# Kernel tuning notes

Hardware: AMD Instinct MI355X
Metric: run time of the kernel (lower is better)

## Reference

```python
import jax, jax.numpy as jnp
import numpy as np

D_MODEL = 1024
D_INNER = 2048   # expand=2
D_STATE = 16
D_CONV = 4
DT_RANK = 64     # ceil(d_model/16)
BATCH = 4
SEQLEN = 2048


def setup_inputs() -> dict:
    key = jax.random.key(0)
    ks = jax.random.split(key, 9)
    f = lambda k, shape, s=0.02: jax.random.normal(k, shape, dtype=jnp.float32) * s
    return {
        "x": jax.random.normal(ks[0], (BATCH, SEQLEN, D_MODEL), dtype=jnp.float32),
        "norm_w": jnp.ones((D_MODEL,), jnp.float32),
        "in_proj_w": f(ks[1], (2 * D_INNER, D_MODEL)),
        "conv_w": f(ks[2], (D_INNER, D_CONV), 0.1),
        "conv_b": f(ks[3], (D_INNER,), 0.1),
        "x_proj_w": f(ks[4], (DT_RANK + 2 * D_STATE, D_INNER)),
        "dt_proj_w": f(ks[5], (D_INNER, DT_RANK), 0.1),
        "dt_proj_b": f(ks[6], (D_INNER,), 0.1),
        "A_log": jnp.log(jnp.tile(jnp.arange(1, D_STATE + 1, dtype=jnp.float32), (D_INNER, 1))),
        "D_param": jnp.ones((D_INNER,), jnp.float32),
        "out_proj_w": f(ks[7], (D_MODEL, D_INNER)),
    }


def _rmsnorm(x, w):
    eps = jnp.finfo(jnp.float32).eps
    var = jnp.mean(x * x, axis=-1, keepdims=True)
    return x * jax.lax.rsqrt(var + eps) * w


def _mamba(x_norm, in_proj_w, conv_w, conv_b, x_proj_w,
           dt_proj_w, dt_proj_b, A_log, D_param, out_proj_w):
    B, L, _ = x_norm.shape
    # input projection -> [B, L, 2*D_INNER], split into x and gate z
    xz = jnp.einsum('bld,ed->ble', x_norm, in_proj_w)
    x_in, z = jnp.split(xz, 2, axis=-1)
    # causal depthwise conv1d (kernel D_CONV, left pad D_CONV-1)
    x_c = jax.lax.conv_general_dilated(
        x_in.transpose(0, 2, 1),                 # [B, D_INNER, L]
        conv_w[:, None, :],                      # [D_INNER, 1, D_CONV]
        window_strides=(1,), padding=[(D_CONV - 1, 0)],
        dimension_numbers=('NCH', 'OIH', 'NCH'),
        feature_group_count=D_INNER,
    ) + conv_b[None, :, None]
    u = jax.nn.silu(x_c.transpose(0, 2, 1))      # [B, L, D_INNER]
    # SSM parameters
    x_dbl = jnp.einsum('bld,ed->ble', u, x_proj_w)  # [B, L, DT_RANK+2*D_STATE]
    dt, B_mat, C_mat = jnp.split(x_dbl, [DT_RANK, DT_RANK + D_STATE], axis=-1)
    dt = jax.nn.softplus(jnp.einsum('blr,dr->bld', dt, dt_proj_w) + dt_proj_b)  # [B,L,D_INNER]
    A = -jnp.exp(A_log)                          # [D_INNER, D_STATE]

    # selective scan over time; state h: [B, D_INNER, D_STATE]
    def step(h, inputs):
        dt_t, B_t, C_t, u_t = inputs             # [B,Dn],[B,S],[B,S],[B,Dn]
        dA = jnp.exp(dt_t[:, :, None] * A)       # [B, Dn, S]
        h = dA * h + (dt_t * u_t)[:, :, None] * B_t[:, None, :]
        y_t = jnp.einsum('bds,bs->bd', h, C_t)
        return h, y_t

    h0 = jnp.zeros((B, D_INNER, D_STATE), x_norm.dtype)
    xs = (dt.transpose(1, 0, 2), B_mat.transpose(1, 0, 2),
          C_mat.transpose(1, 0, 2), u.transpose(1, 0, 2))
    _, ys = jax.lax.scan(step, h0, xs)           # [L, B, D_INNER]
    y = ys.transpose(1, 0, 2) + D_param * u
    y = y * jax.nn.silu(z)
    return jnp.einsum('bld,ed->ble', y, out_proj_w)  # [B, L, D_MODEL]


def reference(x, norm_w, in_proj_w, conv_w, conv_b, x_proj_w,
              dt_proj_w, dt_proj_b, A_log, D_param, out_proj_w):
    x_norm = _rmsnorm(x, norm_w)
    out = _mamba(x_norm, in_proj_w, conv_w, conv_b, x_proj_w,
                 dt_proj_w, dt_proj_b, A_log, D_param, out_proj_w)
    return x + out
```

## Files before the change

kernel.cpp:

```cpp
#include <hip/hip_runtime.h>
#include <hip/hip_bf16.h>
#include <math.h>

#define DM 1024
#define DI 2048
#define DS 16
#define DC 4
#define DR 64
#define NB 4
#define SL 2048
#define BL (NB * SL)
#define DXP (DR + 2 * DS)
#define NC 32
#define CL (SL / NC)

typedef __hip_bfloat16 bf16;
typedef __attribute__((ext_vector_type(8))) short short8;
typedef __attribute__((ext_vector_type(4))) float floatx4;
typedef unsigned int u32;

__device__ __forceinline__ float to_f(float v) { return v; }
__device__ __forceinline__ float to_f(bf16 v) { return __bfloat162float(v); }
template <typename T> __device__ __forceinline__ T from_f(float v);
template <> __device__ __forceinline__ float from_f<float>(float v) { return v; }
template <> __device__ __forceinline__ bf16 from_f<bf16>(float v) { return __float2bfloat16(v); }

__device__ __forceinline__ float bfbits2f(unsigned short u) {
  u32 b = ((u32)u) << 16;
  return __builtin_bit_cast(float, b);
}
__device__ __forceinline__ short f2bfbits(float v) {
  bf16 b = __float2bfloat16(v);
  return __builtin_bit_cast(short, b);
}
__device__ __forceinline__ float fsilu(float v) {
  return v * __builtin_amdgcn_rcpf(1.f + __expf(-v));
}

__device__ __forceinline__ void gload16(const ushort* g, ushort* l) {
  __builtin_amdgcn_global_load_lds((const __attribute__((address_space(1))) void*)g,
                                   (__attribute__((address_space(3))) void*)l,
                                   16, 0, 0);
}

__global__ __launch_bounds__(256) void f2b_k(const float* __restrict__ src,
                                             bf16* __restrict__ dst, int n) {
  int i = blockIdx.x * 256 + threadIdx.x;
  if (i < n) dst[i] = from_f<bf16>(src[i]);
}

__global__ __launch_bounds__(256) void rmsnorm_k(const float* __restrict__ x,
                                                 const float* __restrict__ w,
                                                 bf16* __restrict__ o) {
  int row = blockIdx.x;
  const float* xr = x + (size_t)row * DM;
  float ss = 0.f;
  for (int i = threadIdx.x; i < DM; i += 256) { float v = xr[i]; ss += v * v; }
  for (int off = 32; off > 0; off >>= 1) ss += __shfl_down(ss, off);
  __shared__ float sred[4];
  __shared__ float sscale;
  if ((threadIdx.x & 63) == 0) sred[threadIdx.x >> 6] = ss;
  __syncthreads();
  if (threadIdx.x == 0) {
    float t = sred[0] + sred[1] + sred[2] + sred[3];
    sscale = rsqrtf(t / (float)DM + 1.1920929e-7f);
  }
  __syncthreads();
  float sc = sscale;
  bf16* orow = o + (size_t)row * DM;
  for (int i = threadIdx.x; i < DM; i += 256) orow[i] = from_f<bf16>(xr[i] * sc * w[i]);
}

#define TM 128
#define TN 128
#define TK 32
#define LDK 40
template <int MODE>
__global__ __launch_bounds__(256) void gemm_mfma(const bf16* __restrict__ A,
                                                 const bf16* __restrict__ W,
                                                 int M, int N, int K,
                                                 bf16* __restrict__ Cx,
                                                 bf16* __restrict__ Cz, int nsplit,
                                                 float* __restrict__ Cf,
                                                 const float* __restrict__ R,
                                                 const float* __restrict__ bias) {
  __shared__ ushort Asm[TM][TK];
  __shared__ ushort Bsm[TN][TK];
  int bm = blockIdx.y * TM, bn = blockIdx.x * TN;
  int tid = threadIdx.x;
  int lane = tid & 63, wave = tid >> 6;
  int wm = (wave & 1) * 64, wn = (wave >> 1) * 64;
  int row15 = lane & 15, quad = lane >> 4;

  int srow = lane >> 2;
  int scol = (lane & 3) * 8;
  int s0 = wave * 2, s1 = wave * 2 + 1;

  const ushort* Au = (const ushort*)A;
  const ushort* Wu = (const ushort*)W;
  const ushort* ag0 = Au + (size_t)(bm + s0 * 16 + srow) * K + scol;
  const ushort* ag1 = Au + (size_t)(bm + s1 * 16 + srow) * K + scol;
  const ushort* bg0 = Wu + (size_t)(bn + s0 * 16 + srow) * K + scol;
  const ushort* bg1 = Wu + (size_t)(bn + s1 * 16 + srow) * K + scol;
  ushort* la0 = &Asm[s0 * 16][0];
  ushort* la1 = &Asm[s1 * 16][0];
  ushort* lb0 = &Bsm[s0 * 16][0];
  ushort* lb1 = &Bsm[s1 * 16][0];

  floatx4 acc[4][4] = {};

  for (int k0 = 0; k0 < K; k0 += TK) {
    gload16(ag0 + k0, la0);
    gload16(ag1 + k0, la1);
    gload16(bg0 + k0, lb0);
    gload16(bg1 + k0, lb1);
    __syncthreads();
    short8 a_f[4], b_f[4];
#pragma unroll
    for (int i = 0; i < 4; ++i)
      a_f[i] = *(const short8*)&Asm[wm + i * 16 + row15][quad * 8];
#pragma unroll
    for (int j = 0; j < 4; ++j)
      b_f[j] = *(const short8*)&Bsm[wn + j * 16 + row15][quad * 8];
#pragma unroll
    for (int i = 0; i < 4; ++i)
#pragma unroll
      for (int j = 0; j < 4; ++j)
        acc[i][j] = __builtin_amdgcn_mfma_f32_16x16x32_bf16(a_f[i], b_f[j], acc[i][j], 0, 0, 0);
    __syncthreads();
  }
#pragma unroll
  for (int mi = 0; mi < 4; ++mi) {
#pragma unroll
    for (int ni = 0; ni < 4; ++ni) {
#pragma unroll
      for (int reg = 0; reg < 4; ++reg) {
        int grow = bm + wm + mi * 16 + quad * 4 + reg;
        int gcol = bn + wn + ni * 16 + row15;
        float v = acc[mi][ni][reg];
        if (MODE == 1) {
          if (gcol < nsplit) {
            Cx[(size_t)grow * DI + gcol] = from_f<bf16>(v);
          } else {
            Cz[(size_t)grow * DI + (gcol - nsplit)] = from_f<bf16>(fsilu(v));
          }
        } else if (MODE == 2) {
          size_t o = (size_t)grow * N + gcol;
          Cf[o] = v + R[o];
        } else {
          float t = v + bias[gcol];
          float sp = (t > 20.f) ? t : __logf(1.f + __expf(t));
          Cx[(size_t)grow * N + gcol] = from_f<bf16>(sp);
        }
      }
    }
  }
}

#define XKS 128
__global__ __launch_bounds__(256) void xproj_k(const bf16* __restrict__ u,
                                               const bf16* __restrict__ w,
                                               float* __restrict__ xdbl) {
  __shared__ ushort Asm[128][LDK];
  __shared__ ushort Bsm[96][LDK];
  int kbase = blockIdx.x * XKS;
  int bm = blockIdx.y * 128;
  int tid = threadIdx.x;
  int lane = tid & 63, wave = tid >> 6;
  int row15 = lane & 15, quad = lane >> 4;
  int srow = tid >> 1, skoff = (tid & 1) * 16;

  floatx4 acc[2][6] = {};
  const ushort* Au = (const ushort*)u;
  const ushort* Wu = (const ushort*)w;
  for (int k0 = kbase; k0 < kbase + XKS; k0 += TK) {
    const ushort* ag = Au + (size_t)(bm + srow) * DI + k0 + skoff;
    *(short8*)&Asm[srow][skoff]     = *(const short8*)ag;
    *(short8*)&Asm[srow][skoff + 8] = *(const short8*)(ag + 8);
    if (tid < 192) {
      const ushort* wg = Wu + (size_t)srow * DI + k0 + skoff;
      *(short8*)&Bsm[srow][skoff]     = *(const short8*)wg;
      *(short8*)&Bsm[srow][skoff + 8] = *(const short8*)(wg + 8);
    }
    __syncthreads();
    short8 a_f[2], b_f[6];
#pragma unroll
    for (int i = 0; i < 2; ++i)
      a_f[i] = *(const short8*)&Asm[wave * 32 + i * 16 + row15][quad * 8];
#pragma unroll
    for (int j = 0; j < 6; ++j)
      b_f[j] = *(const short8*)&Bsm[j * 16 + row15][quad * 8];
#pragma unroll
    for (int i = 0; i < 2; ++i)
#pragma unroll
      for (int j = 0; j < 6; ++j)
        acc[i][j] = __builtin_amdgcn_mfma_f32_16x16x32_bf16(a_f[i], b_f[j], acc[i][j], 0, 0, 0);
    __syncthreads();
  }
#pragma unroll
  for (int mi = 0; mi < 2; ++mi)
#pragma unroll
    for (int nj = 0; nj < 6; ++nj)
#pragma unroll
      for (int reg = 0; reg < 4; ++reg) {
        int grow = bm + wave * 32 + mi * 16 + quad * 4 + reg;
        int gcol = nj * 16 + row15;
        atomicAdd(&xdbl[(size_t)grow * DXP + gcol], acc[mi][nj][reg]);
      }
}

__global__ __launch_bounds__(256) void dtex_k(const float* __restrict__ xdbl,
                                              bf16* __restrict__ dtin) {
  int i = blockIdx.x * 256 + threadIdx.x;
  int r = i >> 6, c = i & 63;
  dtin[i] = from_f<bf16>(xdbl[(size_t)r * DXP + c]);
}

#define TSTRIP 8
__global__ __launch_bounds__(256) void conv_silu_k(const bf16* __restrict__ xin,
                                                   const float* __restrict__ cw,
                                                   const float* __restrict__ cb,
                                                   bf16* __restrict__ u) {
  int blk = blockIdx.x;
  int b = blk >> 8;
  int l0 = (blk & 255) * TSTRIP;
  int c0 = threadIdx.x * 8;

  float4 cw4[8];
  const float4* cwp = (const float4*)cw;
#pragma unroll
  for (int j = 0; j < 8; ++j) cw4[j] = cwp[c0 + j];
  float cbv[8];
  {
    float4 cb0 = *(const float4*)&cb[c0];
    float4 cb1 = *(const float4*)&cb[c0 + 4];
    cbv[0] = cb0.x; cbv[1] = cb0.y; cbv[2] = cb0.z; cbv[3] = cb0.w;
    cbv[4] = cb1.x; cbv[5] = cb1.y; cbv[6] = cb1.z; cbv[7] = cb1.w;
  }

  const ushort* base = (const ushort*)xin + ((size_t)(b * SL + l0) * DI + c0);
  ushort* ubase = (ushort*)u + ((size_t)(b * SL + l0) * DI + c0);

  short8 zz = {};
  short8 w0 = zz, w1 = zz, w2 = zz;
  if (l0 >= 3) {
    w0 = *(const short8*)(base - 3 * DI);
    w1 = *(const short8*)(base - 2 * DI);
    w2 = *(const short8*)(base - 1 * DI);
  }
#pragma unroll
  for (int l = 0; l < TSTRIP; ++l) {
    short8 w3 = *(const short8*)(base + (ptrdiff_t)l * DI);
    short8 outv;
#pragma unroll
    for (int j = 0; j < 8; ++j) {
      float a = cbv[j]
              + bfbits2f((unsigned short)w0[j]) * cw4[j].x
              + bfbits2f((unsigned short)w1[j]) * cw4[j].y
              + bfbits2f((unsigned short)w2[j]) * cw4[j].z
              + bfbits2f((unsigned short)w3[j]) * cw4[j].w;
      outv[j] = f2bfbits(fsilu(a));
    }
    *(short8*)(ubase + (ptrdiff_t)l * DI) = outv;
    w0 = w1; w1 = w2; w2 = w3;
  }
}

__global__ __launch_bounds__(256) void scan_p1(const bf16* __restrict__ dts,
                                               const bf16* __restrict__ u,
                                               const float* __restrict__ xdbl,
                                               const float* __restrict__ A_log,
                                               float* __restrict__ Pbuf,
                                               float* __restrict__ Qbuf) {
  int bid = blockIdx.x;
  int b = bid >> 8;
  int c = (bid >> 3) & (NC - 1);
  int d = (bid & 7) * 256 + threadIdx.x;

  float A[DS], h[DS], P[DS];
#pragma unroll
  for (int s = 0; s < DS; ++s) {
    A[s] = -__expf(A_log[d * DS + s]);
    h[s] = 0.f; P[s] = 1.f;
  }
  size_t bl0 = (size_t)b * SL + c * CL;
  size_t base = bl0 * DI + d;
  size_t xb = bl0 * DXP + DR;
  for (int l = 0; l < CL; ++l) {
    float dtv = to_f(dts[base]);
    float uv = to_f(u[base]);
    float du = dtv * uv;
#pragma unroll
    for (int s = 0; s < DS; ++s) {
      float Bv = xdbl[xb + s];
      float dA = __expf(dtv * A[s]);
      h[s] = dA * h[s] + du * Bv;
      P[s] *= dA;
    }
    base += DI;
    xb += DXP;
  }
  size_t o = ((size_t)(b * NC + c) * DS) * DI + d;
#pragma unroll
  for (int s = 0; s < DS; ++s) {
    Pbuf[o + (size_t)s * DI] = P[s];
    Qbuf[o + (size_t)s * DI] = h[s];
  }
}

__global__ __launch_bounds__(256) void scan_p2(float* __restrict__ Pbuf,
                                               float* __restrict__ Qbuf) {
  int bid = blockIdx.x;
  int b = bid >> 7;
  int s = (bid >> 3) & (DS - 1);
  int d = (bid & 7) * 256 + threadIdx.x;
  float h = 0.f;
  for (int c = 0; c < NC; ++c) {
    size_t idx = ((size_t)((b * NC + c) * DS + s)) * DI + d;
    float Pv = Pbuf[idx];
    float qv = Qbuf[idx];
    Qbuf[idx] = h;
    h = Pv * h + qv;
  }
}

__global__ __launch_bounds__(256) void scan_p3(const bf16* __restrict__ dts,
                                               bf16* __restrict__ u,
                                               const float* __restrict__ xdbl,
                                               const float* __restrict__ A_log,
                                               const float* __restrict__ Dp,
                                               const bf16* __restrict__ g,
                                               const float* __restrict__ Qbuf) {
  int bid = blockIdx.x;
  int b = bid >> 8;
  int c = (bid >> 3) & (NC - 1);
  int d = (bid & 7) * 256 + threadIdx.x;

  float A[DS], h[DS];
  size_t o = ((size_t)(b * NC + c) * DS) * DI + d;
#pragma unroll
  for (int s = 0; s < DS; ++s) {
    A[s] = -__expf(A_log[d * DS + s]);
    h[s] = Qbuf[o + (size_t)s * DI];
  }
  float Dd = Dp[d];
  size_t bl0 = (size_t)b * SL + c * CL;
  size_t base = bl0 * DI + d;
  size_t xb = bl0 * DXP + DR;
  for (int l = 0; l < CL; ++l) {
    float dtv = to_f(dts[base]);
    float uv = to_f(u[base]);
    float gv = to_f(g[base]);
    float du = dtv * uv;
    float p0 = 0.f, p1 = 0.f, p2 = 0.f, p3 = 0.f;
#pragma unroll
    for (int s = 0; s < DS; s += 4) {
      float dA0 = __expf(dtv * A[s + 0]);
      float dA1 = __expf(dtv * A[s + 1]);
      float dA2 = __expf(dtv * A[s + 2]);
      float dA3 = __expf(dtv * A[s + 3]);
      h[s + 0] = dA0 * h[s + 0] + du * xdbl[xb + s + 0];
      h[s + 1] = dA1 * h[s + 1] + du * xdbl[xb + s + 1];
      h[s + 2] = dA2 * h[s + 2] + du * xdbl[xb + s + 2];
      h[s + 3] = dA3 * h[s + 3] + du * xdbl[xb + s + 3];
      p0 += h[s + 0] * xdbl[xb + DS + s + 0];
      p1 += h[s + 1] * xdbl[xb + DS + s + 1];
      p2 += h[s + 2] * xdbl[xb + DS + s + 2];
      p3 += h[s + 3] * xdbl[xb + DS + s + 3];
    }
    float yv = ((p0 + p1) + (p2 + p3)) + Dd * uv;
    u[base] = from_f<bf16>(yv * gv);
    base += DI;
    xb += DXP;
  }
}

extern "C" void kernel_launch(void* const* d_in, const int* in_sizes, int n_in,
                              void* d_out, int out_size, void* d_ws, size_t ws_size,
                              hipStream_t stream) {
  const float* x        = (const float*)d_in[0];
  const float* norm_w   = (const float*)d_in[1];
  const float* in_projw = (const float*)d_in[2];
  const float* conv_w   = (const float*)d_in[3];
  const float* conv_b   = (const float*)d_in[4];
  const float* x_projw  = (const float*)d_in[5];
  const float* dt_projw = (const float*)d_in[6];
  const float* dt_projb = (const float*)d_in[7];
  const float* A_log    = (const float*)d_in[8];
  const float* Dp       = (const float*)d_in[9];
  const float* out_projw= (const float*)d_in[10];
  float* out = (float*)d_out;

  char* wsb = (char*)d_ws;
  bf16* x_buf  = (bf16*)wsb;
  bf16* z_buf  = (bf16*)(wsb + (size_t)BL * DI * 2);
  bf16* u_buf  = (bf16*)(wsb + (size_t)BL * DI * 4);
  char* ovl    = wsb + (size_t)BL * DI * 6;
  bf16* ipw_bf = (bf16*)ovl;
  float* xdbl   = (float*)ovl;
  bf16*  xpw_bf = (bf16*)(ovl + 3145728);
  bf16*  dtw_bf = (bf16*)(ovl + 3538944);
  bf16*  dtin_bf= (bf16*)(ovl + 3801088);
  bf16* xnorm_bf = u_buf;
  bf16* dt_buf   = x_buf;
  bf16* opw_bf   = x_buf;
  float* Pbuf = out;
  float* Qbuf = out + (size_t)NB * NC * DS * DI;

  f2b_k<<<(2 * DI * DM) / 256, 256, 0, stream>>>(in_projw, ipw_bf, 2 * DI * DM);
  rmsnorm_k<<<BL, 256, 0, stream>>>(x, norm_w, xnorm_bf);
  gemm_mfma<1><<<dim3(2 * DI / TN, BL / TM), 256, 0, stream>>>(
      xnorm_bf, ipw_bf, BL, 2 * DI, DM, x_buf, z_buf, DI, nullptr, nullptr, nullptr);
  conv_silu_k<<<NB * (SL / TSTRIP), 256, 0, stream>>>(x_buf, conv_w, conv_b, u_buf);
  hipMemsetAsync(xdbl, 0, (size_t)BL * DXP * sizeof(float), stream);
  f2b_k<<<(DXP * DI + 255) / 256, 256, 0, stream>>>(x_projw, xpw_bf, DXP * DI);
  f2b_k<<<(DI * DR) / 256, 256, 0, stream>>>(dt_projw, dtw_bf, DI * DR);
  xproj_k<<<dim3(DI / XKS, BL / 128), 256, 0, stream>>>(u_buf, xpw_bf, xdbl);
  dtex_k<<<(BL * DR) / 256, 256, 0, stream>>>(xdbl, dtin_bf);
  gemm_mfma<3><<<dim3(DI / TN, BL / TM), 256, 0, stream>>>(
      dtin_bf, dtw_bf, BL, DI, DR, dt_buf, nullptr, 0, nullptr, nullptr, dt_projb);
  scan_p1<<<NB * NC * (DI / 256), 256, 0, stream>>>(dt_buf, u_buf, xdbl, A_log, Pbuf, Qbuf);
  scan_p2<<<NB * DS * (DI / 256), 256, 0, stream>>>(Pbuf, Qbuf);
  scan_p3<<<NB * NC * (DI / 256), 256, 0, stream>>>(dt_buf, u_buf, xdbl, A_log, Dp, z_buf, Qbuf);
  f2b_k<<<(DM * DI) / 256, 256, 0, stream>>>(out_projw, opw_bf, DM * DI);
  gemm_mfma<2><<<dim3(DM / TN, BL / TM), 256, 0, stream>>>(
      u_buf, opw_bf, BL, DM, DI, nullptr, nullptr, 0, out, x, nullptr);
}
```

Baseline: 503.3 us.

## Replace in/out projection GEMMs with 256x256 tiled pipelined MFMA kernel

Adds a 512-thread GEMM kernel with 256x256 output tiles, 64-wide K steps, double-buffered LDS filled by direct global-to-LDS loads with swizzled layout, explicit vmcnt waits and barriers interleaved with MFMA quarters, plus a grouped tile swizzle for L2 reuse. It replaces the 128x128 kernel for the input and output projections. The aim is higher arithmetic intensity and overlap of loads with MFMA work. The cost is heavy register and LDS use at one block per CU, and fewer workgroups for the output projection (128 tiles).

New measurement: 489.2 us. 1.03x faster.

```diff
diff --git a/kernel.cpp b/kernel.cpp
--- a/kernel.cpp
+++ b/kernel.cpp
@@ -41,6 +41,14 @@
   __builtin_amdgcn_global_load_lds((const __attribute__((address_space(1))) void*)g,
                                    (__attribute__((address_space(3))) void*)l,
                                    16, 0, 0);
+}
+
+__device__ __forceinline__ void vmw4() { asm volatile("s_waitcnt vmcnt(4)" ::: "memory"); }
+__device__ __forceinline__ void vmw0() { asm volatile("s_waitcnt vmcnt(0)" ::: "memory"); }
+__device__ __forceinline__ void barx() {
+  asm volatile("" ::: "memory");
+  __builtin_amdgcn_s_barrier();
+  asm volatile("" ::: "memory");
 }
 
 __global__ __launch_bounds__(256) void f2b_k(const float* __restrict__ src,
@@ -69,6 +77,132 @@
   float sc = sscale;
   bf16* orow = o + (size_t)row * DM;
   for (int i = threadIdx.x; i < DM; i += 256) orow[i] = from_f<bf16>(xr[i] * sc * w[i]);
+}
+
+template <int MODE>
+__global__ __launch_bounds__(512, 1) void gemm256(const bf16* __restrict__ A,
+                                                  const bf16* __restrict__ W,
+                                                  int M, int N, int K,
+                                                  bf16* __restrict__ Cx,
+                                                  bf16* __restrict__ Cz, int nsplit,
+                                                  float* __restrict__ Cf,
+                                                  const float* __restrict__ R) {
+  __shared__ ushort SH[65536];
+  const int tid = threadIdx.x;
+  const int lane = tid & 63, wv = tid >> 6;
+  const int wr = wv >> 2, wc = wv & 3;
+  const int row15 = lane & 15, quad = lane >> 4;
+
+  int ntm = M >> 8, ntn = N >> 8, nwg = ntm * ntn;
+  int bid = blockIdx.x;
+  int swz = (bid & 7) * (nwg >> 3) + (bid >> 3);
+  int bm0 = (swz % ntm) << 8, bn0 = (swz / ntm) << 8;
+
+  const int nt = K >> 6;
+  const ushort* Au = (const ushort*)A;
+  const ushort* Wu = (const ushort*)W;
+
+  const int w4u = lane ^ (((lane >> 5) & 1) << 1);
+  const int Wsw = (((row15 << 6) | (quad << 4)) ^ (((row15 >> 3) & 1) << 5));
+  const char* SHb = (const char*)SH;
+  const int Abase0 = (wr << 14) + Wsw;
+  const int Abase1 = 32768 + (wr << 14) + Wsw;
+  const int Bbase0 = 65536 + ((wc >> 1) << 14) + ((wc & 1) << 13) + Wsw;
+  const int Bbase1 = Bbase0 + 32768;
+
+  auto stageA = [&](int tt, int half, int buf) {
+    const ushort* g = Au + (size_t)(bm0 + half * 128) * K + tt * 64;
+    char* lds = (char*)SH + (size_t)(buf * 2 + half) * 16384;
+#pragma unroll
+    for (int i = 0; i < 2; ++i) {
+      int sub = wv + i * 8;
+      int r = ((sub >> 1) << 4) | (w4u >> 2);
+      int ce = ((sub & 1) << 5) | ((w4u & 3) << 3);
+      gload16(g + (size_t)r * K + ce, (ushort*)(lds + sub * 1024));
+    }
+  };
+  auto stageB = [&](int tt, int half, int buf) {
+    const ushort* g = Wu + (size_t)(bn0 + half * 128) * K + tt * 64;
+    char* lds = (char*)SH + 65536 + (size_t)(buf * 2 + half) * 16384;
+#pragma unroll
+    for (int i = 0; i < 2; ++i) {
+      int sub = wv + i * 8;
+      int r = ((sub >> 1) << 4) | (w4u >> 2);
+      int ce = ((sub & 1) << 5) | ((w4u & 3) << 3);
+      gload16(g + (size_t)r * K + ce, (ushort*)(lds + sub * 1024));
+    }
+  };
+
+  short8 a_f[4][2], bq[2][2][2];
+  floatx4 acc[8][4] = {};
+
+#define LDA_(base, mh) do { _Pragma("unroll") for (int mi = 0; mi < 4; ++mi) \
+  { _Pragma("unroll") for (int kk = 0; kk < 2; ++kk) \
+    a_f[mi][kk] = *(const short8*)(SHb + (base) + ((((mh)*4 + mi)*2 + kk) << 10)); } } while (0)
+#define LDB_(base, nh) do { _Pragma("unroll") for (int ni = 0; ni < 2; ++ni) \
+  { _Pragma("unroll") for (int kk = 0; kk < 2; ++kk) \
+    bq[nh][ni][kk] = *(const short8*)(SHb + (base) + (((((nh)*2 + ni)*2 + kk)) << 10)); } } while (0)
+#define MM_(mh, nh) do { __builtin_amdgcn_s_setprio(1); \
+  _Pragma("unroll") for (int mi = 0; mi < 4; ++mi) \
+  { _Pragma("unroll") for (int ni = 0; ni < 2; ++ni) \
+    { _Pragma("unroll") for (int kk = 0; kk < 2; ++kk) \
+      acc[(mh)*4+mi][(nh)*2+ni] = __builtin_amdgcn_mfma_f32_16x16x32_bf16( \
+          a_f[mi][kk], bq[nh][ni][kk], acc[(mh)*4+mi][(nh)*2+ni], 0, 0, 0); } } \
+  __builtin_amdgcn_s_setprio(0); } while (0)
+
+#define TILE_(t, AB, BB, curbuf, nxtbuf) do { \
+  int tp1 = (t) + 1, tp2 = (t) + 2; \
+  LDA_(AB, 0); LDB_(BB, 0); \
+  if (tp1 < nt) stageA(tp1, 0, nxtbuf); \
+  barx(); MM_(0, 0); barx(); \
+  LDB_(BB, 1); \
+  if (tp1 < nt) stageA(tp1, 1, nxtbuf); \
+  barx(); MM_(0, 1); barx(); \
+  LDA_(AB, 1); \
+  if (tp2 < nt) stageB(tp2, 0, curbuf); \
+  barx(); MM_(1, 1); barx(); \
+  if (tp2 < nt) stageB(tp2, 1, curbuf); \
+  barx(); MM_(1, 0); \
+  if (tp2 < nt) vmw4(); else vmw0(); \
+  barx(); \
+} while (0)
+
+  stageB(0, 0, 0); stageB(0, 1, 0); stageA(0, 0, 0); stageA(0, 1, 0);
+  stageB(1, 0, 1); stageB(1, 1, 1);
+  vmw4();
+  barx();
+
+  for (int t = 0; t < nt; t += 2) {
+    TILE_(t, Abase0, Bbase0, 0, 1);
+    TILE_(t + 1, Abase1, Bbase1, 1, 0);
+  }
+#undef TILE_
+#undef MM_
+#undef LDB_
+#undef LDA_
+
+#pragma unroll
+  for (int mi8 = 0; mi8 < 8; ++mi8) {
+#pragma unroll
+    for (int ni4 = 0; ni4 < 4; ++ni4) {
+#pragma unroll
+      for (int reg = 0; reg < 4; ++reg) {
+        int grow = bm0 + wr * 128 + mi8 * 16 + quad * 4 + reg;
+        int gcol = bn0 + wc * 64 + ni4 * 16 + row15;
+        float v = acc[mi8][ni4][reg];
+        if (MODE == 1) {
+          if (gcol < nsplit) {
+            Cx[(size_t)grow * DI + gcol] = from_f<bf16>(v);
+          } else {
+            Cz[(size_t)grow * DI + (gcol - nsplit)] = from_f<bf16>(fsilu(v));
+          }
+        } else {
+          size_t o = (size_t)grow * N + gcol;
+          Cf[o] = v + R[o];
+        }
+      }
+    }
+  }
 }
 
 #define TM 128
@@ -409,8 +543,8 @@
 
   f2b_k<<<(2 * DI * DM) / 256, 256, 0, stream>>>(in_projw, ipw_bf, 2 * DI * DM);
   rmsnorm_k<<<BL, 256, 0, stream>>>(x, norm_w, xnorm_bf);
-  gemm_mfma<1><<<dim3(2 * DI / TN, BL / TM), 256, 0, stream>>>(
-      xnorm_bf, ipw_bf, BL, 2 * DI, DM, x_buf, z_buf, DI, nullptr, nullptr, nullptr);
+  gemm256<1><<<(BL / 256) * (2 * DI / 256), 512, 0, stream>>>(
+      xnorm_bf, ipw_bf, BL, 2 * DI, DM, x_buf, z_buf, DI, nullptr, nullptr);
   conv_silu_k<<<NB * (SL / TSTRIP), 256, 0, stream>>>(x_buf, conv_w, conv_b, u_buf);
   hipMemsetAsync(xdbl, 0, (size_t)BL * DXP * sizeof(float), stream);
   f2b_k<<<(DXP * DI + 255) / 256, 256, 0, stream>>>(x_projw, xpw_bf, DXP * DI);
@@ -423,6 +557,6 @@
   scan_p2<<<NB * DS * (DI / 256), 256, 0, stream>>>(Pbuf, Qbuf);
   scan_p3<<<NB * NC * (DI / 256), 256, 0, stream>>>(dt_buf, u_buf, xdbl, A_log, Dp, z_buf, Qbuf);
   f2b_k<<<(DM * DI) / 256, 256, 0, stream>>>(out_projw, opw_bf, DM * DI);
-  gemm_mfma<2><<<dim3(DM / TN, BL / TM), 256, 0, stream>>>(
-      u_buf, opw_bf, BL, DM, DI, nullptr, nullptr, 0, out, x, nullptr);
-}
+  gemm256<2><<<(BL / 256) * (DM / 256), 512, 0, stream>>>(
+      u_buf, opw_bf, BL, DM, DI, nullptr, nullptr, 0, out, x);
+}
```

## Add 256x128 pipelined MFMA GEMM with async LDS loads for in/out projections

Applied to the files above, without the earlier changes.

Introduces a new 512-thread GEMM kernel with 256x128 tiles, K-step 64, double-buffered direct global-to-LDS loads, swizzled LDS layout, explicit vmcnt waits and barriers interleaving staging with MFMA, plus a block-index swizzle for cache locality. It replaces the older 128x128 GEMM for the input and output projections. The aim is to improve MFMA utilisation and hide memory latency in the two largest matmuls. It adds complex hand-scheduled synchronisation that assumes dimensions divisible by the tile sizes.

Result: no change. 503.3 us (+0.0%).

```diff
diff --git a/kernel.cpp b/kernel.cpp
--- a/kernel.cpp
+++ b/kernel.cpp
@@ -41,6 +41,14 @@
   __builtin_amdgcn_global_load_lds((const __attribute__((address_space(1))) void*)g,
                                    (__attribute__((address_space(3))) void*)l,
                                    16, 0, 0);
+}
+
+__device__ __forceinline__ void vmw2() { asm volatile("s_waitcnt vmcnt(2)" ::: "memory"); }
+__device__ __forceinline__ void vmw0() { asm volatile("s_waitcnt vmcnt(0)" ::: "memory"); }
+__device__ __forceinline__ void barx() {
+  asm volatile("" ::: "memory");
+  __builtin_amdgcn_s_barrier();
+  asm volatile("" ::: "memory");
 }
 
 __global__ __launch_bounds__(256) void f2b_k(const float* __restrict__ src,
@@ -69,6 +77,130 @@
   float sc = sscale;
   bf16* orow = o + (size_t)row * DM;
   for (int i = threadIdx.x; i < DM; i += 256) orow[i] = from_f<bf16>(xr[i] * sc * w[i]);
+}
+
+template <int MODE>
+__global__ __launch_bounds__(512, 1) void gemm256(const bf16* __restrict__ A,
+                                                  const bf16* __restrict__ W,
+                                                  int M, int N, int K,
+                                                  bf16* __restrict__ Cx,
+                                                  bf16* __restrict__ Cz, int nsplit,
+                                                  float* __restrict__ Cf,
+                                                  const float* __restrict__ R) {
+  __shared__ ushort SH[49152];
+  const int tid = threadIdx.x;
+  const int lane = tid & 63, wv = tid >> 6;
+  const int wr = wv >> 1, wc = wv & 1;
+  const int row15 = lane & 15, quad = lane >> 4;
+
+  int ntm = M >> 8, ntn = N >> 7, nwg = ntm * ntn;
+  int bid = blockIdx.x;
+  int swz = (bid & 7) * (nwg >> 3) + (bid >> 3);
+  int bm0 = (swz % ntm) << 8, bn0 = (swz / ntm) << 7;
+
+  const int nt = K >> 6;
+  const ushort* Au = (const ushort*)A;
+  const ushort* Wu = (const ushort*)W;
+  const ushort* Ag = Au + (u32)bm0 * (u32)K;
+  const ushort* Bg = Wu + (u32)bn0 * (u32)K;
+
+  const int w4u = lane ^ (((lane >> 5) & 1) << 1);
+  const int sub0 = wv, sub1 = wv + 8;
+  const int r0 = ((sub0 >> 1) << 4) | (w4u >> 2);
+  const int c0 = ((sub0 & 1) << 5) | ((w4u & 3) << 3);
+  const int r1 = ((sub1 >> 1) << 4) | (w4u >> 2);
+  const int c1 = ((sub1 & 1) << 5) | ((w4u & 3) << 3);
+  ushort* shA = (ushort*)SH;
+  ushort* shB = (ushort*)SH + 32768;
+
+  auto stage = [&](const ushort* gbase, int rowoff, int tt, ushort* lbase) {
+    gload16(gbase + (u32)(rowoff + r0) * (u32)K + (u32)(tt * 64 + c0), lbase + (sub0 << 9));
+    gload16(gbase + (u32)(rowoff + r1) * (u32)K + (u32)(tt * 64 + c1), lbase + (sub1 << 9));
+  };
+
+  const int Wsw = (((row15 << 6) | (quad << 4)) ^ (((row15 >> 3) & 1) << 5));
+  const char* SHb = (const char*)SH;
+  const int AB0 = (wr << 13) + Wsw;
+  const int AB1 = 32768 + AB0;
+  const int BB0 = 65536 + (wc << 13) + Wsw;
+  const int BB1 = BB0 + 16384;
+
+  short8 a0[2][2], a1[2][2], bq0A[2][2], bq0B[2][2], bq1[2][2];
+  floatx4 acc[4][4] = {};
+
+#define LDA_(dst, base, mh) do { _Pragma("unroll") for (int i_ = 0; i_ < 2; ++i_) \
+  { _Pragma("unroll") for (int kk = 0; kk < 2; ++kk) \
+    dst[i_][kk] = *(const short8*)(SHb + (base) + ((((mh)*2 + i_)*2 + kk) << 10)); } } while (0)
+#define LDB_(dst, base, nh) do { _Pragma("unroll") for (int j_ = 0; j_ < 2; ++j_) \
+  { _Pragma("unroll") for (int kk = 0; kk < 2; ++kk) \
+    dst[j_][kk] = *(const short8*)(SHb + (base) + ((((nh)*2 + j_)*2 + kk) << 10)); } } while (0)
+#define MM_(aset, bset, mh, nh) do { __builtin_amdgcn_s_setprio(1); \
+  _Pragma("unroll") for (int i_ = 0; i_ < 2; ++i_) \
+  { _Pragma("unroll") for (int j_ = 0; j_ < 2; ++j_) \
+    { _Pragma("unroll") for (int kk = 0; kk < 2; ++kk) \
+      acc[(mh)*2+i_][(nh)*2+j_] = __builtin_amdgcn_mfma_f32_16x16x32_bf16( \
+          aset[i_][kk], bset[j_][kk], acc[(mh)*2+i_][(nh)*2+j_], 0, 0, 0); } } \
+  __builtin_amdgcn_s_setprio(0); } while (0)
+
+#define TILE_(t, ABc, BBc, ABn, BBn, BQU, BQF, CURB, NXTB) do { \
+  int tp1 = (t) + 1, tp2 = (t) + 2; \
+   \
+  LDB_(bq1, BBc, 1); \
+  if (tp1 < nt) stage(Ag, 0, tp1, shA + (NXTB) * 16384); \
+  barx(); MM_(a0, BQU, 0, 0); barx(); \
+   \
+  LDA_(a1, ABc, 1); \
+  if (tp1 < nt) stage(Ag, 128, tp1, shA + (NXTB) * 16384 + 8192); \
+  barx(); MM_(a0, bq1, 0, 1); barx(); \
+   \
+  if (tp2 < nt) stage(Bg, 0, tp2, shB + (CURB) * 8192); \
+  barx(); MM_(a1, bq1, 1, 1); \
+  if (tp2 < nt) vmw2(); else vmw0(); \
+  barx(); \
+   \
+  if (tp1 < nt) { LDA_(a0, ABn, 0); LDB_(BQF, BBn, 0); } \
+  barx(); MM_(a1, BQU, 1, 0); barx(); \
+} while (0)
+
+  stage(Bg, 0, 0, shB);
+  stage(Ag, 0, 0, shA);
+  stage(Ag, 128, 0, shA + 8192);
+  if (nt > 1) { stage(Bg, 0, 1, shB + 8192); vmw2(); } else { vmw0(); }
+  barx();
+  LDA_(a0, AB0, 0);
+  LDB_(bq0A, BB0, 0);
+
+  for (int t = 0; t < nt; t += 2) {
+    TILE_(t,     AB0, BB0, AB1, BB1, bq0A, bq0B, 0, 1);
+    TILE_(t + 1, AB1, BB1, AB0, BB0, bq0B, bq0A, 1, 0);
+  }
+#undef TILE_
+#undef MM_
+#undef LDB_
+#undef LDA_
+
+#pragma unroll
+  for (int mi = 0; mi < 4; ++mi) {
+#pragma unroll
+    for (int ni = 0; ni < 4; ++ni) {
+#pragma unroll
+      for (int reg = 0; reg < 4; ++reg) {
+        int grow = bm0 + wr * 64 + mi * 16 + quad * 4 + reg;
+        int gcol = bn0 + wc * 64 + ni * 16 + row15;
+        float v = acc[mi][ni][reg];
+        if (MODE == 1) {
+          if (gcol < nsplit) {
+            Cx[(u32)grow * DI + (u32)gcol] = from_f<bf16>(v);
+          } else {
+            Cz[(u32)grow * DI + (u32)(gcol - nsplit)] = from_f<bf16>(fsilu(v));
+          }
+        } else {
+          u32 o = (u32)grow * (u32)N + (u32)gcol;
+          Cf[o] = v + R[o];
+        }
+      }
+    }
+  }
 }
 
 #define TM 128
@@ -409,8 +541,8 @@
 
   f2b_k<<<(2 * DI * DM) / 256, 256, 0, stream>>>(in_projw, ipw_bf, 2 * DI * DM);
   rmsnorm_k<<<BL, 256, 0, stream>>>(x, norm_w, xnorm_bf);
-  gemm_mfma<1><<<dim3(2 * DI / TN, BL / TM), 256, 0, stream>>>(
-      xnorm_bf, ipw_bf, BL, 2 * DI, DM, x_buf, z_buf, DI, nullptr, nullptr, nullptr);
+  gemm256<1><<<(BL / 256) * (2 * DI / 128), 512, 0, stream>>>(
+      xnorm_bf, ipw_bf, BL, 2 * DI, DM, x_buf, z_buf, DI, nullptr, nullptr);
   conv_silu_k<<<NB * (SL / TSTRIP), 256, 0, stream>>>(x_buf, conv_w, conv_b, u_buf);
   hipMemsetAsync(xdbl, 0, (size_t)BL * DXP * sizeof(float), stream);
   f2b_k<<<(DXP * DI + 255) / 256, 256, 0, stream>>>(x_projw, xpw_bf, DXP * DI);
@@ -423,6 +555,6 @@
   scan_p2<<<NB * DS * (DI / 256), 256, 0, stream>>>(Pbuf, Qbuf);
   scan_p3<<<NB * NC * (DI / 256), 256, 0, stream>>>(dt_buf, u_buf, xdbl, A_log, Dp, z_buf, Qbuf);
   f2b_k<<<(DM * DI) / 256, 256, 0, stream>>>(out_projw, opw_bf, DM * DI);
-  gemm_mfma<2><<<dim3(DM / TN, BL / TM), 256, 0, stream>>>(
-      u_buf, opw_bf, BL, DM, DI, nullptr, nullptr, 0, out, x, nullptr);
-}
+  gemm256<2><<<(BL / 256) * (DM / 128), 512, 0, stream>>>(
+      u_buf, opw_bf, BL, DM, DI, nullptr, nullptr, 0, out, x);
+}
```
